# Kernel optimization log

Hardware: AMD Instinct MI355X
Metric: run time of the kernel (lower is better)

## Reference

```python
import jax, jax.numpy as jnp
import numpy as np

LN_EPS = 1e-5


def _gru_scan(xg, w_hh, b_hh, H, reverse):
    # xg: [T, B, 3H] precomputed input-gate activations (W_ih x + b_ih)
    B = xg.shape[1]
    h0 = jnp.zeros((B, H), xg.dtype)

    def step(h, xt):
        hg = h @ w_hh.T + b_hh                      # [B, 3H]
        r = jax.nn.sigmoid(xt[:, :H] + hg[:, :H])
        z = jax.nn.sigmoid(xt[:, H:2 * H] + hg[:, H:2 * H])
        n = jnp.tanh(xt[:, 2 * H:] + r * hg[:, 2 * H:])
        h = (1.0 - z) * n + z * h
        return h, h

    _, ys = jax.lax.scan(step, h0, xg, reverse=reverse)
    return ys                                       # [T, B, H]


def setup_inputs() -> dict:
    key = jax.random.key(0)
    ks = jax.random.split(key, 12)
    B, T, I, H = 32, 1000, 512, 512
    s = 1.0 / np.sqrt(H)
    u = lambda k, shape: jax.random.uniform(k, shape, jnp.float32, -s, s)
    return {
        "x": jax.random.normal(ks[0], (B, T, I), jnp.float32),
        "ln_gamma": jnp.ones((I,), jnp.float32),
        "ln_beta": jnp.zeros((I,), jnp.float32),
        "w_ih_f": u(ks[1], (3 * H, I)),
        "w_hh_f": u(ks[2], (3 * H, H)),
        "b_ih_f": u(ks[3], (3 * H,)),
        "b_hh_f": u(ks[4], (3 * H,)),
        "w_ih_b": u(ks[5], (3 * H, I)),
        "w_hh_b": u(ks[6], (3 * H, H)),
        "b_ih_b": u(ks[7], (3 * H,)),
        "b_hh_b": u(ks[8], (3 * H,)),
    }


def reference(x, ln_gamma, ln_beta, w_ih_f, w_hh_f, b_ih_f, b_hh_f,
              w_ih_b, w_hh_b, b_ih_b, b_hh_b):
    H = w_hh_f.shape[1]
    # LayerNorm over last dim
    mu = jnp.mean(x, axis=-1, keepdims=True)
    var = jnp.var(x, axis=-1, keepdims=True)
    xn = (x - mu) * jax.lax.rsqrt(var + LN_EPS) * ln_gamma + ln_beta
    # ReLU6
    xn = jnp.clip(xn, 0.0, 6.0)
    # batch_first -> time-major [T, B, I]
    xt = jnp.transpose(xn, (1, 0, 2))
    # Precompute input projections for both directions
    xg_f = xt @ w_ih_f.T + b_ih_f                   # [T, B, 3H]
    xg_b = xt @ w_ih_b.T + b_ih_b
    yf = _gru_scan(xg_f, w_hh_f, b_hh_f, H, reverse=False)
    yb = _gru_scan(xg_b, w_hh_b, b_hh_b, H, reverse=True)
    y = jnp.concatenate([yf, yb], axis=-1)          # [T, B, 2H]
    # dropout treated as identity (deterministic reference)
    return jnp.transpose(y, (1, 0, 2))              # [B, T, 2H]
```

## Files before the change

### kernel.cpp

```cpp
#include <hip/hip_runtime.h>


typedef _Float16 half8   __attribute__((ext_vector_type(8)));
typedef _Float16 half2_  __attribute__((ext_vector_type(2)));
typedef float    floatx4 __attribute__((ext_vector_type(4)));
typedef float    floatx2 __attribute__((ext_vector_type(2)));
typedef unsigned int uintx4 __attribute__((ext_vector_type(4)));

#define T_LEN 1000
#define NB    32
#define DIM   512

#define XN_OFF   0
#define HB_OFF   32768000
#define CTR_OFF  32899072
#define WS_NEED  32899328

__device__ __forceinline__ float bf2f(unsigned short b) {
  unsigned int u = ((unsigned int)b) << 16; float f; __builtin_memcpy(&f, &u, 4); return f;
}
__device__ __forceinline__ unsigned short f2bf(float f) {
  unsigned int u; __builtin_memcpy(&u, &f, 4);
  u = (u + 0x7FFFu + ((u >> 16) & 1u)) >> 16;
  return (unsigned short)u;
}

__global__ void init_kernel(unsigned int* ws32) {
  const int base = HB_OFF / 4;
  const int n    = (WS_NEED - HB_OFF) / 4;
  for (int i = blockIdx.x * blockDim.x + threadIdx.x; i < n; i += gridDim.x * blockDim.x)
    ws32[base + i] = 0u;
}

__global__ __launch_bounds__(256) void ln_kernel(const void* __restrict__ xin,
                                                 const void* __restrict__ gam,
                                                 const void* __restrict__ bet,
                                                 unsigned short* __restrict__ xn) {
  const bool bf = (((const unsigned int*)gam)[0] != 0x3F800000u);
  const int w = threadIdx.x >> 6, l = threadIdx.x & 63;
  const int row = blockIdx.x * 4 + w;
  const int b = row / T_LEN, t = row - b * T_LEN;

  float v[8], g[8], be[8];
  if (bf) {
    const unsigned int* xp = (const unsigned int*)xin + (row * 512 + l * 8) / 2;
    uintx4 r4 = *(const uintx4*)xp;
    uintx4 g4 = *(const uintx4*)((const unsigned int*)gam + l * 4);
    uintx4 b4 = *(const uintx4*)((const unsigned int*)bet + l * 4);
#pragma unroll
    for (int j = 0; j < 4; ++j) {
      v[2*j]   = bf2f((unsigned short)(r4[j] & 0xFFFFu));
      v[2*j+1] = bf2f((unsigned short)(r4[j] >> 16));
      g[2*j]   = bf2f((unsigned short)(g4[j] & 0xFFFFu));
      g[2*j+1] = bf2f((unsigned short)(g4[j] >> 16));
      be[2*j]  = bf2f((unsigned short)(b4[j] & 0xFFFFu));
      be[2*j+1] = bf2f((unsigned short)(b4[j] >> 16));
    }
  } else {
    const float* xp = (const float*)xin + (size_t)row * 512 + l * 8;
    floatx4 a0 = *(const floatx4*)xp;
    floatx4 a1 = *(const floatx4*)(xp + 4);
    const float* gp = (const float*)gam + l * 8;
    const float* bp = (const float*)bet + l * 8;
#pragma unroll
    for (int j = 0; j < 4; ++j) {
      v[j] = a0[j]; v[4+j] = a1[j];
      g[j] = gp[j]; g[4+j] = gp[4+j];
      be[j] = bp[j]; be[4+j] = bp[4+j];
    }
  }

  float s1 = 0.f, s2 = 0.f;
#pragma unroll
  for (int j = 0; j < 8; ++j) { s1 += v[j]; s2 += v[j] * v[j]; }
#pragma unroll
  for (int m = 1; m < 64; m <<= 1) { s1 += __shfl_xor(s1, m); s2 += __shfl_xor(s2, m); }
  const float mean = s1 * (1.f / 512.f);
  const float var  = s2 * (1.f / 512.f) - mean * mean;
  const float rstd = rsqrtf(var + 1e-5f);

  unsigned int out[4];
#pragma unroll
  for (int j = 0; j < 4; ++j) {
    float f0 = (v[2*j]   - mean) * rstd * g[2*j]   + be[2*j];
    float f1 = (v[2*j+1] - mean) * rstd * g[2*j+1] + be[2*j+1];
    f0 = fminf(fmaxf(f0, 0.f), 6.f);
    f1 = fminf(fmaxf(f1, 0.f), 6.f);
    half2_ hp = { (_Float16)f0, (_Float16)f1 };
    __builtin_memcpy(&out[j], &hp, 4);
  }
  *(uintx4*)(xn + ((size_t)(t * 32 + b) * 512 + l * 8)) = *(uintx4*)out;
}

#define SMEM_BYTES 125312

__global__ __launch_bounds__(256, 1) void gru_kernel(
    const void* __restrict__ wihF, const void* __restrict__ whhF,
    const void* __restrict__ bihF, const void* __restrict__ bhhF,
    const void* __restrict__ wihB, const void* __restrict__ whhB,
    const void* __restrict__ bihB, const void* __restrict__ bhhB,
    const void* __restrict__ gam,
    const unsigned short* __restrict__ xn,
    unsigned short* __restrict__ hb,
    unsigned int* __restrict__ ctr,
    void* __restrict__ yout) {
  extern __shared__ char smem[];
  _Float16* wih = (_Float16*)smem;
  _Float16* whh = (_Float16*)(smem + 49152);
  float* part = (float*)(smem + 98304);
  float* hown = (float*)(smem + 122880);
  float* bihs = (float*)(smem + 124928);
  float* bhhs = (float*)(smem + 125120);

  const bool bf = (((const unsigned int*)gam)[0] != 0x3F800000u);
  const int tid = threadIdx.x;
  const int w = tid >> 6, l = tid & 63, quad = l >> 4, lan = l & 15;
  const int dir = blockIdx.x >> 5, wg = blockIdx.x & 31, c0 = wg * 16;

  const void* Wg[2] = { dir ? wihB : wihF, dir ? whhB : whhF };
  const void* Bg[2] = { dir ? bihB : bihF, dir ? bhhB : bhhF };

  for (int idx = tid; idx < 6144; idx += 256) {
    const int mat = idx / 3072;
    const int r = idx - mat * 3072;
    const int nt = r >> 10, s = (r >> 6) & 15, ln = r & 63;
    const int row = nt * 512 + c0 + (ln & 15);
    const int k0 = s * 32 + (ln >> 4) * 8;
    float tmp[8];
    if (bf) {
      const unsigned int* p = (const unsigned int*)Wg[mat] + (row * 512 + k0) / 2;
      uintx4 r4 = *(const uintx4*)p;
#pragma unroll
      for (int j = 0; j < 4; ++j) {
        tmp[2*j]   = bf2f((unsigned short)(r4[j] & 0xFFFFu));
        tmp[2*j+1] = bf2f((unsigned short)(r4[j] >> 16));
      }
    } else {
      const float* p = (const float*)Wg[mat] + (size_t)row * 512 + k0;
      floatx4 a0 = *(const floatx4*)p;
      floatx4 a1 = *(const floatx4*)(p + 4);
#pragma unroll
      for (int j = 0; j < 4; ++j) { tmp[j] = a0[j]; tmp[4+j] = a1[j]; }
    }
    _Float16* dst = (mat ? whh : wih) + ((size_t)((nt * 16 + s) * 64 + ln)) * 8;
#pragma unroll
    for (int j = 0; j < 8; ++j) dst[j] = (_Float16)tmp[j];
  }
  if (tid < 96) {
    const int mat = tid / 48, i = tid % 48, g_ = i >> 4, c = i & 15;
    const int gi = g_ * 512 + c0 + c;
    float v = bf ? bf2f(((const unsigned short*)Bg[mat])[gi]) : ((const float*)Bg[mat])[gi];
    (mat ? bhhs : bihs)[i] = v;
  }
  for (int i = tid; i < 512; i += 256) hown[i] = 0.f;
  __syncthreads();

  unsigned int* myctr = ctr + dir * 16;
  const int kh = w & 1;
  unsigned short* hb_d = hb + dir * 2 * 16384;
  const _Float16* wb = (w < 2) ? wih : whh;

  for (int t = 0; t < T_LEN; ++t) {
    const int tt = dir ? (T_LEN - 1 - t) : t;
    const int cur = t & 1, nxt = cur ^ 1;

    floatx4 acc[2][3];
#pragma unroll
    for (int mt = 0; mt < 2; ++mt)
#pragma unroll
      for (int nt = 0; nt < 3; ++nt) acc[mt][nt] = (floatx4){0.f, 0.f, 0.f, 0.f};

    if (w < 2) {
      const _Float16* A = (const _Float16*)xn + (size_t)tt * 16384;
      half8 av[2][8];
#pragma unroll
      for (int si = 0; si < 8; ++si) {
        const int s = kh * 8 + si, k0 = s * 32 + quad * 8;
        av[0][si] = *(const half8*)(A + (lan * 512 + k0));
        av[1][si] = *(const half8*)(A + ((16 + lan) * 512 + k0));
      }
#pragma unroll
      for (int si = 0; si < 8; ++si) {
        const int s = kh * 8 + si;
#pragma unroll
        for (int nt = 0; nt < 3; ++nt) {
          half8 bfr = *(const half8*)(wb + ((size_t)((nt * 16 + s) * 64 + l)) * 8);
          acc[0][nt] = __builtin_amdgcn_mfma_f32_16x16x32_f16(av[0][si], bfr, acc[0][nt], 0, 0, 0);
          acc[1][nt] = __builtin_amdgcn_mfma_f32_16x16x32_f16(av[1][si], bfr, acc[1][nt], 0, 0, 0);
        }
      }
    } else {
      const unsigned long long* A = (const unsigned long long*)(hb_d + cur * 16384);
      union HU { unsigned long long q[2]; half8 h; };
      HU u[2][8];
#pragma unroll
      for (int si = 0; si < 8; ++si) {
        const int s = kh * 8 + si, k0 = s * 32 + quad * 8;
        const unsigned long long* p0 = A + (lan * 512 + k0) / 4;
        const unsigned long long* p1 = A + ((16 + lan) * 512 + k0) / 4;
        u[0][si].q[0] = __hip_atomic_load(p0,     __ATOMIC_RELAXED, __HIP_MEMORY_SCOPE_AGENT);
        u[0][si].q[1] = __hip_atomic_load(p0 + 1, __ATOMIC_RELAXED, __HIP_MEMORY_SCOPE_AGENT);
        u[1][si].q[0] = __hip_atomic_load(p1,     __ATOMIC_RELAXED, __HIP_MEMORY_SCOPE_AGENT);
        u[1][si].q[1] = __hip_atomic_load(p1 + 1, __ATOMIC_RELAXED, __HIP_MEMORY_SCOPE_AGENT);
      }
#pragma unroll
      for (int si = 0; si < 8; ++si) {
        const int s = kh * 8 + si;
#pragma unroll
        for (int nt = 0; nt < 3; ++nt) {
          half8 bfr = *(const half8*)(wb + ((size_t)((nt * 16 + s) * 64 + l)) * 8);
          acc[0][nt] = __builtin_amdgcn_mfma_f32_16x16x32_f16(u[0][si].h, bfr, acc[0][nt], 0, 0, 0);
          acc[1][nt] = __builtin_amdgcn_mfma_f32_16x16x32_f16(u[1][si].h, bfr, acc[1][nt], 0, 0, 0);
        }
      }
    }

#pragma unroll
    for (int mt = 0; mt < 2; ++mt)
#pragma unroll
      for (int nt = 0; nt < 3; ++nt) {
        float* p = part + ((w * 6 + mt * 3 + nt) << 8);
#pragma unroll
        for (int r = 0; r < 4; ++r) p[(quad * 4 + r) * 16 + lan] = acc[mt][nt][r];
      }
    __syncthreads();

    {
      const int b = tid >> 3, cp = tid & 7;
      const int mt = b >> 4, mr = b & 15;
      float hv[2];
#pragma unroll
      for (int e = 0; e < 2; ++e) {
        const int c = cp * 2 + e;
        const int o = mr * 16 + c;
#define PT(W_, NT_) part[(((W_) * 6 + mt * 3 + (NT_)) << 8) + o]
        const float xr = PT(0, 0) + PT(1, 0) + bihs[c];
        const float xz = PT(0, 1) + PT(1, 1) + bihs[16 + c];
        const float xg = PT(0, 2) + PT(1, 2) + bihs[32 + c];
        const float hr = PT(2, 0) + PT(3, 0) + bhhs[c];
        const float hz = PT(2, 1) + PT(3, 1) + bhhs[16 + c];
        const float hg = PT(2, 2) + PT(3, 2) + bhhs[32 + c];
#undef PT
        const float rr = 1.f / (1.f + __expf(-(xr + hr)));
        const float zz = 1.f / (1.f + __expf(-(xz + hz)));
        float a = xg + rr * hg;
        a = fminf(fmaxf(a, -15.f), 15.f);
        const float e2 = __expf(2.f * a);
        const float nn = (e2 - 1.f) / (e2 + 1.f);
        const float hp = hown[b * 16 + c];
        const float hvv = (1.f - zz) * nn + zz * hp;
        hown[b * 16 + c] = hvv;
        hv[e] = hvv;
      }
      half2_ pk = { (_Float16)hv[0], (_Float16)hv[1] };
      unsigned int pu; __builtin_memcpy(&pu, &pk, 4);
      unsigned int* hdst = (unsigned int*)(hb_d + nxt * 16384 + b * 512 + c0 + cp * 2);
      __hip_atomic_store(hdst, pu, __ATOMIC_RELAXED, __HIP_MEMORY_SCOPE_AGENT);
      const size_t yo = ((size_t)b * T_LEN + tt) * 1024 + dir * 512 + c0 + cp * 2;
      if (bf) {
        unsigned int yp = (unsigned int)f2bf(hv[0]) | ((unsigned int)f2bf(hv[1]) << 16);
        *(unsigned int*)((unsigned short*)yout + yo) = yp;
      } else {
        *(floatx2*)((float*)yout + yo) = (floatx2){hv[0], hv[1]};
      }
    }

    if (t < T_LEN - 1) {
      __syncthreads();
      if (tid == 0) {
        __hip_atomic_fetch_add(myctr, 1u, __ATOMIC_RELAXED, __HIP_MEMORY_SCOPE_AGENT);
        const unsigned int tgt = 32u * (unsigned int)(t + 1);
        while (__hip_atomic_load(myctr, __ATOMIC_RELAXED, __HIP_MEMORY_SCOPE_AGENT) < tgt)
          __builtin_amdgcn_s_sleep(1);
      }
      __syncthreads();
    }
  }
}

extern "C" void kernel_launch(void* const* d_in, const int* in_sizes, int n_in,
                              void* d_out, int out_size, void* d_ws, size_t ws_size,
                              hipStream_t stream) {
  if (ws_size < (size_t)WS_NEED) return;

  (void)hipFuncSetAttribute((const void*)gru_kernel,
                            hipFuncAttributeMaxDynamicSharedMemorySize, 131072);

  const void* x   = d_in[0];
  const void* gam = d_in[1];
  const void* bet = d_in[2];
  const void* wihF = d_in[3]; const void* whhF = d_in[4];
  const void* bihF = d_in[5]; const void* bhhF = d_in[6];
  const void* wihB = d_in[7]; const void* whhB = d_in[8];
  const void* bihB = d_in[9]; const void* bhhB = d_in[10];

  unsigned short* xnp = (unsigned short*)((char*)d_ws + XN_OFF);
  unsigned short* hbp = (unsigned short*)((char*)d_ws + HB_OFF);
  unsigned int*   cp  = (unsigned int*)((char*)d_ws + CTR_OFF);

  init_kernel<<<64, 256, 0, stream>>>((unsigned int*)d_ws);
  ln_kernel<<<8000, 256, 0, stream>>>(x, gam, bet, xnp);
  gru_kernel<<<64, 256, SMEM_BYTES, stream>>>(wihF, whhF, bihF, bhhF,
                                              wihB, whhB, bihB, bhhB,
                                              gam, xnp, hbp, cp, d_out);
}
```

Baseline: 5.337 ms.

## Replace global counter barrier with step-tagged hidden state and register-resident weights

Each hidden-state element is now stored as a 64-bit word that carries the step number, so consumer waves spin on the data itself instead of on a shared atomic counter with two block barriers per step. Weight fragments move from LDS into registers, partial sums are double-buffered in LDS so one barrier per step suffices, and the previous hidden value stays in registers. This removes the global atomic fetch-add, the sleep-poll and extra syncs from the serial per-step critical path. In exchange the hidden-state traffic doubles, register pressure rises sharply (48 half8 weight fragments plus 64 polled words), and correctness depends on the relaxed-ordering polling being safe.

```diff
diff --git a/kernel.cpp b/kernel.cpp
--- a/kernel.cpp
+++ b/kernel.cpp
@@ -8,13 +8,11 @@
 typedef unsigned int uintx4 __attribute__((ext_vector_type(4)));
 
 #define T_LEN 1000
-#define NB    32
 #define DIM   512
 
 #define XN_OFF   0
-#define HB_OFF   32768000
-#define CTR_OFF  32899072
-#define WS_NEED  32899328
+#define HT_OFF   32768000
+#define WS_NEED  33030144
 
 __device__ __forceinline__ float bf2f(unsigned short b) {
   unsigned int u = ((unsigned int)b) << 16; float f; __builtin_memcpy(&f, &u, 4); return f;
@@ -25,11 +23,11 @@
   return (unsigned short)u;
 }
 
-__global__ void init_kernel(unsigned int* ws32) {
-  const int base = HB_OFF / 4;
-  const int n    = (WS_NEED - HB_OFF) / 4;
+__global__ void init_kernel(unsigned long long* ws64) {
+  const int base = HT_OFF / 8;
+  const int n    = (WS_NEED - HT_OFF) / 8;
   for (int i = blockIdx.x * blockDim.x + threadIdx.x; i < n; i += gridDim.x * blockDim.x)
-    ws32[base + i] = 0u;
+    ws64[base + i] = 0ull;
 }
 
 __global__ __launch_bounds__(256) void ln_kernel(const void* __restrict__ xin,
@@ -92,7 +90,7 @@
   *(uintx4*)(xn + ((size_t)(t * 32 + b) * 512 + l * 8)) = *(uintx4*)out;
 }
 
-#define SMEM_BYTES 125312
+#define SMEM_BYTES 49536
 
 __global__ __launch_bounds__(256, 1) void gru_kernel(
     const void* __restrict__ wihF, const void* __restrict__ whhF,
@@ -101,68 +99,72 @@
     const void* __restrict__ bihB, const void* __restrict__ bhhB,
     const void* __restrict__ gam,
     const unsigned short* __restrict__ xn,
-    unsigned short* __restrict__ hb,
-    unsigned int* __restrict__ ctr,
+    unsigned long long* __restrict__ hb,
     void* __restrict__ yout) {
   extern __shared__ char smem[];
-  _Float16* wih = (_Float16*)smem;
-  _Float16* whh = (_Float16*)(smem + 49152);
-  float* part = (float*)(smem + 98304);
-  float* hown = (float*)(smem + 122880);
-  float* bihs = (float*)(smem + 124928);
-  float* bhhs = (float*)(smem + 125120);
+  float* part = (float*)smem;
+  float* bihs = (float*)(smem + 49152);
+  float* bhhs = (float*)(smem + 49344);
 
   const bool bf = (((const unsigned int*)gam)[0] != 0x3F800000u);
   const int tid = threadIdx.x;
   const int w = tid >> 6, l = tid & 63, quad = l >> 4, lan = l & 15;
   const int dir = blockIdx.x >> 5, wg = blockIdx.x & 31, c0 = wg * 16;
-
-  const void* Wg[2] = { dir ? wihB : wihF, dir ? whhB : whhF };
-  const void* Bg[2] = { dir ? bihB : bihF, dir ? bhhB : bhhF };
-
-  for (int idx = tid; idx < 6144; idx += 256) {
-    const int mat = idx / 3072;
-    const int r = idx - mat * 3072;
-    const int nt = r >> 10, s = (r >> 6) & 15, ln = r & 63;
-    const int row = nt * 512 + c0 + (ln & 15);
-    const int k0 = s * 32 + (ln >> 4) * 8;
-    float tmp[8];
-    if (bf) {
-      const unsigned int* p = (const unsigned int*)Wg[mat] + (row * 512 + k0) / 2;
-      uintx4 r4 = *(const uintx4*)p;
-#pragma unroll
-      for (int j = 0; j < 4; ++j) {
-        tmp[2*j]   = bf2f((unsigned short)(r4[j] & 0xFFFFu));
-        tmp[2*j+1] = bf2f((unsigned short)(r4[j] >> 16));
-      }
-    } else {
-      const float* p = (const float*)Wg[mat] + (size_t)row * 512 + k0;
-      floatx4 a0 = *(const floatx4*)p;
-      floatx4 a1 = *(const floatx4*)(p + 4);
-#pragma unroll
-      for (int j = 0; j < 4; ++j) { tmp[j] = a0[j]; tmp[4+j] = a1[j]; }
-    }
-    _Float16* dst = (mat ? whh : wih) + ((size_t)((nt * 16 + s) * 64 + ln)) * 8;
-#pragma unroll
-    for (int j = 0; j < 8; ++j) dst[j] = (_Float16)tmp[j];
-  }
+  const int kh = w & 1;
+
+  const void* Wih = dir ? wihB : wihF;
+  const void* Whh = dir ? whhB : whhF;
+  const void* Bih = dir ? bihB : bihF;
+  const void* Bhh = dir ? bhhB : bhhF;
+
+  half8 wfrag[3][8];
+  {
+    const void* Wm = (w < 2) ? Wih : Whh;
+    const int col = c0 + lan;
+    const int kq  = quad * 8;
+#pragma unroll
+    for (int nt = 0; nt < 3; ++nt)
+#pragma unroll
+      for (int si = 0; si < 8; ++si) {
+        const int s = kh * 8 + si;
+        const int row = nt * 512 + col;
+        const int k0 = s * 32 + kq;
+        half8 hh;
+        if (bf) {
+          const unsigned int* p = (const unsigned int*)Wm + (row * 512 + k0) / 2;
+          uintx4 r4 = *(const uintx4*)p;
+#pragma unroll
+          for (int j = 0; j < 4; ++j) {
+            hh[2*j]   = (_Float16)bf2f((unsigned short)(r4[j] & 0xFFFFu));
+            hh[2*j+1] = (_Float16)bf2f((unsigned short)(r4[j] >> 16));
+          }
+        } else {
+          const float* p = (const float*)Wm + (size_t)row * 512 + k0;
+          floatx4 a0 = *(const floatx4*)p;
+          floatx4 a1 = *(const floatx4*)(p + 4);
+#pragma unroll
+          for (int j = 0; j < 4; ++j) { hh[j] = (_Float16)a0[j]; hh[4+j] = (_Float16)a1[j]; }
+        }
+        wfrag[nt][si] = hh;
+      }
+  }
+
   if (tid < 96) {
     const int mat = tid / 48, i = tid % 48, g_ = i >> 4, c = i & 15;
     const int gi = g_ * 512 + c0 + c;
-    float v = bf ? bf2f(((const unsigned short*)Bg[mat])[gi]) : ((const float*)Bg[mat])[gi];
+    const void* Bm = mat ? Bhh : Bih;
+    float v = bf ? bf2f(((const unsigned short*)Bm)[gi]) : ((const float*)Bm)[gi];
     (mat ? bhhs : bihs)[i] = v;
   }
-  for (int i = tid; i < 512; i += 256) hown[i] = 0.f;
-  __syncthreads();
-
-  unsigned int* myctr = ctr + dir * 16;
-  const int kh = w & 1;
-  unsigned short* hb_d = hb + dir * 2 * 16384;
-  const _Float16* wb = (w < 2) ? wih : whh;
+
+  const int cb = tid >> 3, cp = tid & 7, cmt = cb >> 4, cmr = cb & 15;
+  float hpv0 = 0.f, hpv1 = 0.f;
+
+  unsigned long long* hT = hb + (size_t)dir * 2 * 32 * 256;
 
   for (int t = 0; t < T_LEN; ++t) {
     const int tt = dir ? (T_LEN - 1 - t) : t;
-    const int cur = t & 1, nxt = cur ^ 1;
+    float* pb = part + (t & 1) * 6144;
 
     floatx4 acc[2][3];
 #pragma unroll
@@ -172,45 +174,53 @@
 
     if (w < 2) {
       const _Float16* A = (const _Float16*)xn + (size_t)tt * 16384;
-      half8 av[2][8];
+      half8 av0[8], av1[8];
 #pragma unroll
       for (int si = 0; si < 8; ++si) {
-        const int s = kh * 8 + si, k0 = s * 32 + quad * 8;
-        av[0][si] = *(const half8*)(A + (lan * 512 + k0));
-        av[1][si] = *(const half8*)(A + ((16 + lan) * 512 + k0));
-      }
+        const int k0 = (kh * 8 + si) * 32 + quad * 8;
+        av0[si] = *(const half8*)(A + (lan * 512 + k0));
+        av1[si] = *(const half8*)(A + ((16 + lan) * 512 + k0));
+      }
+#pragma unroll
+      for (int si = 0; si < 8; ++si)
+#pragma unroll
+        for (int nt = 0; nt < 3; ++nt) {
+          acc[0][nt] = __builtin_amdgcn_mfma_f32_16x16x32_f16(av0[si], wfrag[nt][si], acc[0][nt], 0, 0, 0);
+          acc[1][nt] = __builtin_amdgcn_mfma_f32_16x16x32_f16(av1[si], wfrag[nt][si], acc[1][nt], 0, 0, 0);
+        }
+    } else {
+      const unsigned long long* hbuf = hT + (size_t)(t & 1) * 8192;
+      const unsigned int tgt = (unsigned int)t;
+      unsigned long long q[64];
+      int ok;
+      do {
+#pragma unroll
+        for (int si = 0; si < 8; ++si) {
+          const int s = kh * 8 + si;
+          const unsigned long long* p0 = hbuf + lan * 256 + s * 16 + quad * 4;
+#pragma unroll
+          for (int j = 0; j < 4; ++j) {
+            q[si * 8 + j]     = __hip_atomic_load(p0 + j,        __ATOMIC_RELAXED, __HIP_MEMORY_SCOPE_AGENT);
+            q[si * 8 + 4 + j] = __hip_atomic_load(p0 + 4096 + j, __ATOMIC_RELAXED, __HIP_MEMORY_SCOPE_AGENT);
+          }
+        }
+        ok = 1;
+#pragma unroll
+        for (int i = 0; i < 64; ++i) ok &= ((unsigned int)(q[i] >> 32) == tgt) ? 1 : 0;
+      } while (__all(ok) == 0);
+
 #pragma unroll
       for (int si = 0; si < 8; ++si) {
-        const int s = kh * 8 + si;
+        union HU { unsigned int d[4]; half8 h; } a0, a1;
+#pragma unroll
+        for (int j = 0; j < 4; ++j) {
+          a0.d[j] = (unsigned int)q[si * 8 + j];
+          a1.d[j] = (unsigned int)q[si * 8 + 4 + j];
+        }
 #pragma unroll
         for (int nt = 0; nt < 3; ++nt) {
-          half8 bfr = *(const half8*)(wb + ((size_t)((nt * 16 + s) * 64 + l)) * 8);
-          acc[0][nt] = __builtin_amdgcn_mfma_f32_16x16x32_f16(av[0][si], bfr, acc[0][nt], 0, 0, 0);
-          acc[1][nt] = __builtin_amdgcn_mfma_f32_16x16x32_f16(av[1][si], bfr, acc[1][nt], 0, 0, 0);
-        }
-      }
-    } else {
-      const unsigned long long* A = (const unsigned long long*)(hb_d + cur * 16384);
-      union HU { unsigned long long q[2]; half8 h; };
-      HU u[2][8];
-#pragma unroll
-      for (int si = 0; si < 8; ++si) {
-        const int s = kh * 8 + si, k0 = s * 32 + quad * 8;
-        const unsigned long long* p0 = A + (lan * 512 + k0) / 4;
-        const unsigned long long* p1 = A + ((16 + lan) * 512 + k0) / 4;
-        u[0][si].q[0] = __hip_atomic_load(p0,     __ATOMIC_RELAXED, __HIP_MEMORY_SCOPE_AGENT);
-        u[0][si].q[1] = __hip_atomic_load(p0 + 1, __ATOMIC_RELAXED, __HIP_MEMORY_SCOPE_AGENT);
-        u[1][si].q[0] = __hip_atomic_load(p1,     __ATOMIC_RELAXED, __HIP_MEMORY_SCOPE_AGENT);
-        u[1][si].q[1] = __hip_atomic_load(p1 + 1, __ATOMIC_RELAXED, __HIP_MEMORY_SCOPE_AGENT);
-      }
-#pragma unroll
-      for (int si = 0; si < 8; ++si) {
-        const int s = kh * 8 + si;
-#pragma unroll
-        for (int nt = 0; nt < 3; ++nt) {
-          half8 bfr = *(const half8*)(wb + ((size_t)((nt * 16 + s) * 64 + l)) * 8);
-          acc[0][nt] = __builtin_amdgcn_mfma_f32_16x16x32_f16(u[0][si].h, bfr, acc[0][nt], 0, 0, 0);
-          acc[1][nt] = __builtin_amdgcn_mfma_f32_16x16x32_f16(u[1][si].h, bfr, acc[1][nt], 0, 0, 0);
+          acc[0][nt] = __builtin_amdgcn_mfma_f32_16x16x32_f16(a0.h, wfrag[nt][si], acc[0][nt], 0, 0, 0);
+          acc[1][nt] = __builtin_amdgcn_mfma_f32_16x16x32_f16(a1.h, wfrag[nt][si], acc[1][nt], 0, 0, 0);
         }
       }
     }
@@ -219,21 +229,23 @@
     for (int mt = 0; mt < 2; ++mt)
 #pragma unroll
       for (int nt = 0; nt < 3; ++nt) {
-        float* p = part + ((w * 6 + mt * 3 + nt) << 8);
+        float* p = pb + ((w * 6 + mt * 3 + nt) << 8);
 #pragma unroll
         for (int r = 0; r < 4; ++r) p[(quad * 4 + r) * 16 + lan] = acc[mt][nt][r];
       }
-    __syncthreads();
+
+    __builtin_amdgcn_sched_barrier(0);
+    asm volatile("s_waitcnt lgkmcnt(0)" ::: "memory");
+    __builtin_amdgcn_s_barrier();
+    __builtin_amdgcn_sched_barrier(0);
 
     {
-      const int b = tid >> 3, cp = tid & 7;
-      const int mt = b >> 4, mr = b & 15;
       float hv[2];
 #pragma unroll
       for (int e = 0; e < 2; ++e) {
         const int c = cp * 2 + e;
-        const int o = mr * 16 + c;
-#define PT(W_, NT_) part[(((W_) * 6 + mt * 3 + (NT_)) << 8) + o]
+        const int o = cmr * 16 + c;
+#define PT(W_, NT_) pb[(((W_) * 6 + cmt * 3 + (NT_)) << 8) + o]
         const float xr = PT(0, 0) + PT(1, 0) + bihs[c];
         const float xz = PT(0, 1) + PT(1, 1) + bihs[16 + c];
         const float xg = PT(0, 2) + PT(1, 2) + bihs[32 + c];
@@ -247,16 +259,18 @@
         a = fminf(fmaxf(a, -15.f), 15.f);
         const float e2 = __expf(2.f * a);
         const float nn = (e2 - 1.f) / (e2 + 1.f);
-        const float hp = hown[b * 16 + c];
+        const float hp = e ? hpv1 : hpv0;
         const float hvv = (1.f - zz) * nn + zz * hp;
-        hown[b * 16 + c] = hvv;
+        if (e) hpv1 = hvv; else hpv0 = hvv;
         hv[e] = hvv;
       }
       half2_ pk = { (_Float16)hv[0], (_Float16)hv[1] };
       unsigned int pu; __builtin_memcpy(&pu, &pk, 4);
-      unsigned int* hdst = (unsigned int*)(hb_d + nxt * 16384 + b * 512 + c0 + cp * 2);
-      __hip_atomic_store(hdst, pu, __ATOMIC_RELAXED, __HIP_MEMORY_SCOPE_AGENT);
-      const size_t yo = ((size_t)b * T_LEN + tt) * 1024 + dir * 512 + c0 + cp * 2;
+      const unsigned long long qv =
+          (unsigned long long)pu | ((unsigned long long)(unsigned int)(t + 1) << 32);
+      __hip_atomic_store(hT + (size_t)((t + 1) & 1) * 8192 + cb * 256 + wg * 8 + cp,
+                         qv, __ATOMIC_RELAXED, __HIP_MEMORY_SCOPE_AGENT);
+      const size_t yo = ((size_t)cb * T_LEN + tt) * 1024 + dir * 512 + c0 + cp * 2;
       if (bf) {
         unsigned int yp = (unsigned int)f2bf(hv[0]) | ((unsigned int)f2bf(hv[1]) << 16);
         *(unsigned int*)((unsigned short*)yout + yo) = yp;
@@ -264,17 +278,6 @@
         *(floatx2*)((float*)yout + yo) = (floatx2){hv[0], hv[1]};
       }
     }
-
-    if (t < T_LEN - 1) {
-      __syncthreads();
-      if (tid == 0) {
-        __hip_atomic_fetch_add(myctr, 1u, __ATOMIC_RELAXED, __HIP_MEMORY_SCOPE_AGENT);
-        const unsigned int tgt = 32u * (unsigned int)(t + 1);
-        while (__hip_atomic_load(myctr, __ATOMIC_RELAXED, __HIP_MEMORY_SCOPE_AGENT) < tgt)
-          __builtin_amdgcn_s_sleep(1);
-      }
-      __syncthreads();
-    }
   }
 }
 
@@ -284,7 +287,7 @@
   if (ws_size < (size_t)WS_NEED) return;
 
   (void)hipFuncSetAttribute((const void*)gru_kernel,
-                            hipFuncAttributeMaxDynamicSharedMemorySize, 131072);
+                            hipFuncAttributeMaxDynamicSharedMemorySize, 65536);
 
   const void* x   = d_in[0];
   const void* gam = d_in[1];
@@ -294,13 +297,12 @@
   const void* wihB = d_in[7]; const void* whhB = d_in[8];
   const void* bihB = d_in[9]; const void* bhhB = d_in[10];
 
-  unsigned short* xnp = (unsigned short*)((char*)d_ws + XN_OFF);
-  unsigned short* hbp = (unsigned short*)((char*)d_ws + HB_OFF);
-  unsigned int*   cp  = (unsigned int*)((char*)d_ws + CTR_OFF);
-
-  init_kernel<<<64, 256, 0, stream>>>((unsigned int*)d_ws);
+  unsigned short*      xnp = (unsigned short*)((char*)d_ws + XN_OFF);
+  unsigned long long*  hbp = (unsigned long long*)((char*)d_ws + HT_OFF);
+
+  init_kernel<<<16, 256, 0, stream>>>((unsigned long long*)d_ws);
   ln_kernel<<<8000, 256, 0, stream>>>(x, gam, bet, xnp);
   gru_kernel<<<64, 256, SMEM_BYTES, stream>>>(wihF, whhF, bihF, bhhF,
                                               wihB, whhB, bihB, bhhB,
-                                              gam, xnp, hbp, cp, d_out);
-}
+                                              gam, xnp, hbp, d_out);
+}
```

Result: slower. 7.928 ms (+48.6%).
